# Kernel tuning notes

Measured on AMD Instinct MI355X. Metric: run time of the kernel, lower is better.

## Reference

```python
import jax, jax.numpy as jnp
import numpy as np

D_MODEL = 1024
D_KV = 64
N_HEADS = 16
INNER = N_HEADS * D_KV
EPS = 1e-6


def setup_inputs() -> dict:
    key = jax.random.key(0)
    ks = jax.random.split(key, 8)
    B, SQ, SKV = 2, 2048, 4096
    hidden_states = jax.random.normal(ks[0], (B, SQ, D_MODEL), dtype=jnp.float32)
    key_value_states = jax.random.normal(ks[1], (B, SKV, D_MODEL), dtype=jnp.float32)
    attention_mask = jnp.zeros((B, 1, 1, SKV), dtype=jnp.float32)
    # nn.Linear(in, out, bias=False): y = x @ W.T; store W as [in, out] here
    s = 0.02
    Wq = jax.random.normal(ks[2], (D_MODEL, INNER), dtype=jnp.float32) * s
    Wk = jax.random.normal(ks[3], (D_MODEL, INNER), dtype=jnp.float32) * s
    Wv = jax.random.normal(ks[4], (D_MODEL, INNER), dtype=jnp.float32) * s
    Wo = jax.random.normal(ks[5], (INNER, D_MODEL), dtype=jnp.float32) * s
    ln_weight = jnp.ones((D_MODEL,), dtype=jnp.float32)
    return {
        "hidden_states": hidden_states,
        "key_value_states": key_value_states,
        "attention_mask": attention_mask,
        "ln_weight": ln_weight,
        "Wq": Wq,
        "Wk": Wk,
        "Wv": Wv,
        "Wo": Wo,
    }


def _t5_rmsnorm(x, w, eps=EPS):
    # no mean subtraction, variance in fp32
    var = jnp.mean(jnp.square(x.astype(jnp.float32)), axis=-1, keepdims=True)
    return w * (x * jax.lax.rsqrt(var + eps)).astype(x.dtype)


def reference(hidden_states, key_value_states, attention_mask, ln_weight, Wq, Wk, Wv, Wo):
    B, SQ, _ = hidden_states.shape
    SKV = key_value_states.shape[1]
    normed = _t5_rmsnorm(hidden_states, ln_weight)

    # projections -> [B, H, S, Dk]
    q = (normed @ Wq).reshape(B, SQ, N_HEADS, D_KV).transpose(0, 2, 1, 3)
    k = (key_value_states @ Wk).reshape(B, SKV, N_HEADS, D_KV).transpose(0, 2, 1, 3)
    v = (key_value_states @ Wv).reshape(B, SKV, N_HEADS, D_KV).transpose(0, 2, 1, 3)

    # T5: NO 1/sqrt(d) scaling
    scores = jnp.einsum("bhqd,bhkd->bhqk", q, k) + attention_mask
    attn = jax.nn.softmax(scores.astype(jnp.float32), axis=-1).astype(scores.dtype)
    ctx = jnp.einsum("bhqk,bhkd->bhqd", attn, v)
    ctx = ctx.transpose(0, 2, 1, 3).reshape(B, SQ, INNER)
    attn_out = ctx @ Wo
    return hidden_states + attn_out
```

## Files before the change

### kernel.cpp

```cpp
#include <hip/hip_runtime.h>

typedef unsigned short u16;
typedef unsigned int u32;
typedef __attribute__((ext_vector_type(4))) float f32x4;
typedef __attribute__((ext_vector_type(8))) short short8;
typedef __attribute__((ext_vector_type(4))) short short4v;

#define BB   2
#define SQL  2048
#define SKVL 4096
#define DM   1024
#define NH   16
#define DK   64
#define L2E  1.44269504f

#if __has_builtin(__builtin_amdgcn_exp2f)
#define EXP2(x) __builtin_amdgcn_exp2f(x)
#else
#define EXP2(x) exp2f(x)
#endif

#define MFMA32(a, b, c) __builtin_amdgcn_mfma_f32_16x16x32_bf16(a, b, c, 0, 0, 0)

__device__ __forceinline__ u16 f2bf(float f) {
  union { float f; unsigned u; } v; v.f = f;
  unsigned r = v.u + 0x7fff + ((v.u >> 16) & 1);
  return (u16)(r >> 16);
}

__device__ __forceinline__ short4v pack4(float p0, float p1, float p2, float p3) {
  union { float f; u32 u; } a, b, c, d;
  a.f = p0; b.f = p1; c.f = p2; d.f = p3;
  union { uint2 v; short4v s; } r;
  r.v.x = __builtin_amdgcn_perm(b.u + 0x8000u, a.u + 0x8000u, 0x07060302);
  r.v.y = __builtin_amdgcn_perm(d.u + 0x8000u, c.u + 0x8000u, 0x07060302);
  return r.s;
}

__device__ __forceinline__ void gload16(const void* g, void* lds) {
  __builtin_amdgcn_global_load_lds(
      (const __attribute__((address_space(1))) unsigned int*)g,
      (__attribute__((address_space(3))) unsigned int*)lds, 16, 0, 0);
}

__global__ void pre_kernel(const float* __restrict__ hidden, const float* __restrict__ lnw,
                           const float* __restrict__ kvs,
                           const float* __restrict__ Wq, const float* __restrict__ Wk,
                           const float* __restrict__ Wv, const float* __restrict__ Wo,
                           u16* __restrict__ normed, u16* __restrict__ kvb,
                           u16* __restrict__ Wqt, u16* __restrict__ Wkt,
                           u16* __restrict__ Wvt, u16* __restrict__ Wot) {
  __shared__ float red[4];
  __shared__ float tile[32][33];
  int bid = blockIdx.x, t = threadIdx.x;
  if (bid < 4096) {
    int row = bid;
    float4 v = ((const float4*)(hidden + (size_t)row * DM))[t];
    float ss = v.x * v.x + v.y * v.y + v.z * v.z + v.w * v.w;
#pragma unroll
    for (int m = 32; m >= 1; m >>= 1) ss += __shfl_xor(ss, m, 64);
    int lane = t & 63, wv = t >> 6;
    if (lane == 0) red[wv] = ss;
    __syncthreads();
    float total = red[0] + red[1] + red[2] + red[3];
    float scale = rsqrtf(total * (1.0f / DM) + 1e-6f);
    float4 g = ((const float4*)lnw)[t];
    ushort4 o;
    o.x = f2bf(v.x * scale * g.x);
    o.y = f2bf(v.y * scale * g.y);
    o.z = f2bf(v.z * scale * g.z);
    o.w = f2bf(v.w * scale * g.w);
    ((ushort4*)(normed + (size_t)row * DM))[t] = o;
  } else if (bid < 12288) {
    int i = (bid - 4096) * 256 + t;
    float4 v = ((const float4*)kvs)[i];
    ushort4 o;
    o.x = f2bf(v.x); o.y = f2bf(v.y); o.z = f2bf(v.z); o.w = f2bf(v.w);
    ((ushort4*)kvb)[i] = o;
  } else {
    int g = bid - 12288;
    int z = g >> 10;
    const float* W = (z == 0) ? Wq : (z == 1) ? Wk : (z == 2) ? Wv : Wo;
    u16* Wt = (z == 0) ? Wqt : (z == 1) ? Wkt : (z == 2) ? Wvt : Wot;
    int xx = g & 31, yy = (g >> 5) & 31;
    int tx = t & 31, ty = t >> 5;
    int k0 = yy * 32, n0 = xx * 32;
#pragma unroll
    for (int i = 0; i < 4; i++)
      tile[ty + i * 8][tx] = W[(size_t)(k0 + ty + i * 8) * DM + n0 + tx];
    __syncthreads();
#pragma unroll
    for (int i = 0; i < 4; i++)
      Wt[(size_t)(n0 + ty + i * 8) * DM + k0 + tx] = f2bf(tile[tx][ty + i * 8]);
  }
}

__global__ void proj_kernel(const u16* __restrict__ normed, const u16* __restrict__ kvb,
                            const u16* __restrict__ Wqt, const u16* __restrict__ Wkt,
                            const u16* __restrict__ Wvt,
                            u16* __restrict__ Qb, u16* __restrict__ Kbf,
                            u16* __restrict__ Vtb) {
  const int K = 1024;
  __shared__ __align__(16) u16 Al[128 * 32];
  __shared__ __align__(16) u16 Bl[128 * 32];
  int tid = threadIdx.x, lane = tid & 63, w = tid >> 6;
  int l15 = lane & 15, quad = lane >> 4;
  int wy = w >> 1, wx = w & 1;

  int bid = blockIdx.x;
  int mode;
  const u16 *A, *Bt;
  int tm, tn;
  if (bid < 256) { mode = 0; A = normed; Bt = Wqt; tm = (bid & 31) * 128; tn = (bid >> 5) * 128; }
  else if (bid < 768) { mode = 1; A = kvb; Bt = Wkt; int kid = bid - 256; tm = (kid & 63) * 128; tn = (kid >> 6) * 128; }
  else { mode = 2; A = Wvt; Bt = kvb; int vid = bid - 768; tm = (vid & 7) * 128; tn = (vid >> 3) * 128; }

  f32x4 acc[4][4] = {};
  for (int k0 = 0; k0 < K; k0 += 32) {
    __syncthreads();
#pragma unroll
    for (int r = 0; r < 2; r++) {
      int mg = w * 2 + r;
      gload16(A + (size_t)(tm + mg * 16 + l15) * K + k0 + quad * 8, &Al[mg * 512]);
      gload16(Bt + (size_t)(tn + mg * 16 + l15) * K + k0 + quad * 8, &Bl[mg * 512]);
    }
    __syncthreads();
    short8 af[4], bfr[4];
#pragma unroll
    for (int i = 0; i < 4; i++) {
      af[i] = *(const short8*)&Al[((wy * 4 + i) * 64 + lane) * 8];
      bfr[i] = *(const short8*)&Bl[((wx * 4 + i) * 64 + lane) * 8];
    }
#pragma unroll
    for (int mt = 0; mt < 4; mt++)
#pragma unroll
      for (int nt = 0; nt < 4; nt++)
        acc[mt][nt] = MFMA32(af[mt], bfr[nt], acc[mt][nt]);
  }

#pragma unroll
  for (int mt = 0; mt < 4; mt++) {
    int m0 = tm + wy * 64 + mt * 16 + quad * 4;
#pragma unroll
    for (int nt = 0; nt < 4; nt++) {
      int n = tn + wx * 64 + nt * 16 + l15;
      if (mode == 0) {
#pragma unroll
        for (int r = 0; r < 4; r++)
          Qb[(size_t)(m0 + r) * 1024 + n] = f2bf(acc[mt][nt][r] * L2E);
      } else if (mode == 1) {
#pragma unroll
        for (int r = 0; r < 4; r++)
          Kbf[(size_t)(m0 + r) * 1024 + n] = f2bf(acc[mt][nt][r]);
      } else {
        int b = n >> 12, skv = n & 4095;
        int t32 = skv >> 5, p = skv & 31;
        int s = ((p >> 2) & 3) * 8 + ((p >> 4) & 1) * 4 + (p & 3);
        int h = m0 >> 6, d0 = m0 & 63;
        size_t base = (size_t)((b * NH + h) * 128 + t32) * 2048
                    + (size_t)(d0 >> 4) * 512 + (size_t)(s >> 3) * 128 + (s & 7);
#pragma unroll
        for (int r = 0; r < 4; r++)
          Vtb[base + (size_t)((d0 & 15) + r) * 8] = f2bf(acc[mt][nt][r]);
      }
    }
  }
}

__global__ __launch_bounds__(256, 2) void flash_kernel(
    const u16* __restrict__ Qp, const u16* __restrict__ Kp, const u16* __restrict__ Vtb,
    const float* __restrict__ mask, u16* __restrict__ ctx) {
  __shared__ __align__(16) char smem[65536];
  u16* Kbuf = (u16*)smem;
  u16* Vbuf = (u16*)(smem + 32768);
  float* Ox = (float*)smem;
  float* Ll = (float*)(smem + 32768);

  int tid = threadIdx.x, lane = tid & 63, w = tid >> 6;
  int l15 = lane & 15, quad = lane >> 4;
  int grp = w >> 1, wg = w & 1;

  int lid = blockIdx.y * 16 + blockIdx.x;
  int xcd = lid & 7, slot = lid >> 3;
  int bh = xcd * 4 + (slot >> 4);
  int qb = slot & 15;
  int b = bh >> 4, h = bh & 15;
  int q0 = qb * 128 + wg * 64;

  short8 qf[4][2];
#pragma unroll
  for (int mt = 0; mt < 4; mt++)
#pragma unroll
    for (int kf = 0; kf < 2; kf++)
      qf[mt][kf] = *(const short8*)(Qp + (size_t)(b * SQL + q0 + mt * 16 + l15) * DM +
                                    h * DK + kf * 32 + quad * 8);

  f32x4 of[4][4] = {};
  f32x4 la[4] = {};
  const short8 ones8 = {0x3F80, 0x3F80, 0x3F80, 0x3F80, 0x3F80, 0x3F80, 0x3F80, 0x3F80};

  const size_t vblob = (size_t)(b * NH + h) * 262144;
  const float* mrow = mask + (size_t)b * SKVL;

  auto stage = [&](int tileIdx, int buf) {
    int kv0 = tileIdx * 64;
    u16* Kd = Kbuf + (buf * 2 + grp) * 4096;
    u16* Vd = Vbuf + (buf * 2 + grp) * 4096;
#pragma unroll
    for (int r = 0; r < 4; r++) {
      int u = wg * 4 + r;
      int kt = u >> 1, kf = u & 1;
      gload16(Kp + (size_t)(b * SKVL + kv0 + kt * 16 + l15) * DM + h * DK + kf * 32 + quad * 8,
              &Kd[u * 512]);
      gload16(Vtb + vblob + (size_t)tileIdx * 4096 + u * 512 + lane * 8, &Vd[u * 512]);
    }
  };

  f32x4 mlc[4], mln[4];
  {
    int kv0 = grp * 64;
#pragma unroll
    for (int kt = 0; kt < 4; kt++)
      mlc[kt] = *(const f32x4*)(mrow + kv0 + kt * 16 + quad * 4) * L2E;
  }
  stage(grp, 0);

  union PU { short8 v8; short4v h2[2]; };

  for (int it = 0; it < 32; ++it) {
    __syncthreads();
    if (it + 1 < 32) {
      stage((it + 1) * 2 + grp, (it + 1) & 1);
      int kvn = ((it + 1) * 2 + grp) * 64;
#pragma unroll
      for (int kt = 0; kt < 4; kt++)
        mln[kt] = *(const f32x4*)(mrow + kvn + kt * 16 + quad * 4) * L2E;
    }
    const u16* Kg = Kbuf + ((it & 1) * 2 + grp) * 4096;
    const u16* Vg = Vbuf + ((it & 1) * 2 + grp) * 4096;

#pragma unroll
    for (int ktp = 0; ktp < 2; ktp++) {
      PU paf[4];
#pragma unroll
      for (int kth = 0; kth < 2; kth++) {
        int kt = ktp * 2 + kth;
        short8 k0 = *(const short8*)&Kg[((kt * 2 + 0) * 64 + lane) * 8];
        short8 k1 = *(const short8*)&Kg[((kt * 2 + 1) * 64 + lane) * 8];
#pragma unroll
        for (int mt = 0; mt < 4; mt++) {
          f32x4 st = mlc[kt];
          st = MFMA32(k0, qf[mt][0], st);
          st = MFMA32(k1, qf[mt][1], st);
          paf[mt].h2[kth] = pack4(EXP2(st[0]), EXP2(st[1]), EXP2(st[2]), EXP2(st[3]));
        }
      }
#pragma unroll
      for (int mt = 0; mt < 4; mt++)
        la[mt] = MFMA32(paf[mt].v8, ones8, la[mt]);
#pragma unroll
      for (int nt = 0; nt < 4; nt++) {
        short8 vv = *(const short8*)&Vg[ktp * 2048 + (nt * 64 + lane) * 8];
#pragma unroll
        for (int mt = 0; mt < 4; mt++)
          of[mt][nt] = MFMA32(paf[mt].v8, vv, of[mt][nt]);
      }
    }
#pragma unroll
    for (int kt = 0; kt < 4; kt++) mlc[kt] = mln[kt];
  }

  __syncthreads();
  if (grp == 1) {
#pragma unroll
    for (int mt = 0; mt < 4; mt++) {
#pragma unroll
      for (int nt = 0; nt < 4; nt++)
#pragma unroll
        for (int r = 0; r < 4; r++)
          Ox[(wg * 64 + mt * 16 + quad * 4 + r) * 64 + nt * 16 + l15] = of[mt][nt][r];
      if (l15 == 0)
#pragma unroll
        for (int r = 0; r < 4; r++) Ll[wg * 64 + mt * 16 + quad * 4 + r] = la[mt][r];
    }
  }
  __syncthreads();
  if (grp == 0) {
#pragma unroll
    for (int mt = 0; mt < 4; mt++)
#pragma unroll
      for (int r = 0; r < 4; r++) {
        int ql = wg * 64 + mt * 16 + quad * 4 + r;
        float inv = 1.0f / (la[mt][r] + Ll[ql]);
        int q = qb * 128 + ql;
#pragma unroll
        for (int nt = 0; nt < 4; nt++) {
          float ov = of[mt][nt][r] + Ox[ql * 64 + nt * 16 + l15];
          ctx[(size_t)(b * SQL + q) * DM + h * DK + nt * 16 + l15] = f2bf(ov * inv);
        }
      }
  }
}

__global__ void ogemm_kernel(const u16* __restrict__ A, const u16* __restrict__ Bt,
                             float* __restrict__ C, const float* __restrict__ resid) {
  const int K = 1024;
  __shared__ __align__(16) u16 Al[128 * 32];
  __shared__ __align__(16) u16 Bl[128 * 32];
  int tid = threadIdx.x, lane = tid & 63, w = tid >> 6;
  int l15 = lane & 15, quad = lane >> 4;
  int wy = w >> 1, wx = w & 1;
  int tm = blockIdx.x * 128, tn = blockIdx.y * 128;
  f32x4 acc[4][4] = {};

  for (int k0 = 0; k0 < K; k0 += 32) {
    __syncthreads();
#pragma unroll
    for (int r = 0; r < 2; r++) {
      int mg = w * 2 + r;
      gload16(A + (size_t)(tm + mg * 16 + l15) * K + k0 + quad * 8, &Al[mg * 512]);
      gload16(Bt + (size_t)(tn + mg * 16 + l15) * K + k0 + quad * 8, &Bl[mg * 512]);
    }
    __syncthreads();
    short8 af[4], bfr[4];
#pragma unroll
    for (int i = 0; i < 4; i++) {
      af[i] = *(const short8*)&Al[((wy * 4 + i) * 64 + lane) * 8];
      bfr[i] = *(const short8*)&Bl[((wx * 4 + i) * 64 + lane) * 8];
    }
#pragma unroll
    for (int mt = 0; mt < 4; mt++)
#pragma unroll
      for (int nt = 0; nt < 4; nt++)
        acc[mt][nt] = MFMA32(af[mt], bfr[nt], acc[mt][nt]);
  }

#pragma unroll
  for (int mt = 0; mt < 4; mt++) {
    int m0 = tm + wy * 64 + mt * 16 + quad * 4;
#pragma unroll
    for (int nt = 0; nt < 4; nt++) {
      int n = tn + wx * 64 + nt * 16 + l15;
#pragma unroll
      for (int r = 0; r < 4; r++) {
        size_t idx = (size_t)(m0 + r) * 1024 + n;
        C[idx] = resid[idx] + acc[mt][nt][r];
      }
    }
  }
}

extern "C" void kernel_launch(void* const* d_in, const int* in_sizes, int n_in,
                              void* d_out, int out_size, void* d_ws, size_t ws_size,
                              hipStream_t stream) {
  const float* hidden = (const float*)d_in[0];
  const float* kvs    = (const float*)d_in[1];
  const float* mask   = (const float*)d_in[2];
  const float* lnw    = (const float*)d_in[3];
  const float* Wq     = (const float*)d_in[4];
  const float* Wk     = (const float*)d_in[5];
  const float* Wv     = (const float*)d_in[6];
  const float* Wo     = (const float*)d_in[7];
  char* ws = (char*)d_ws;

  u16* normed = (u16*)(ws + 0);
  u16* kvb    = (u16*)(ws + 8388608);
  u16* Wqt    = (u16*)(ws + 25165824);
  u16* Wkt    = (u16*)(ws + 27262976);
  u16* Wvt    = (u16*)(ws + 29360128);
  u16* Wot    = (u16*)(ws + 31457280);
  u16* Qb     = (u16*)(ws + 33554432);
  u16* Kbf    = (u16*)(ws + 41943040);
  u16* Vtb    = (u16*)(ws + 58720256);
  u16* ctxb   = (u16*)(ws + 75497472);

  pre_kernel<<<16384, 256, 0, stream>>>(hidden, lnw, kvs, Wq, Wk, Wv, Wo,
                                        normed, kvb, Wqt, Wkt, Wvt, Wot);
  proj_kernel<<<1280, 256, 0, stream>>>(normed, kvb, Wqt, Wkt, Wvt, Qb, Kbf, Vtb);
  flash_kernel<<<dim3(SQL / 128, BB * NH), 256, 0, stream>>>(Qb, Kbf, Vtb, mask, ctxb);
  ogemm_kernel<<<dim3(32, 8), 256, 0, stream>>>(ctxb, Wot, (float*)d_out, hidden);
}
```

Measured before the change: 323.6 us.

## Fuse K and V projections sharing A tile, enlarge proj blocks to 512 threads

The projection kernel now computes K and V in the same block, loading each key_value tile once and multiplying it against both Wk and Wv. The V projection is no longer computed as a transposed GEMM, and its output is scattered into the flash layout from the same accumulator positions. Blocks grow to 512 threads with 256x128 tiles for K/V and 128x128 tiles for Q, giving 512 blocks in total. The aim is to halve A-tile traffic for K/V and to reduce the block count. The cost is higher register pressure (two accumulator sets) and uncoalesced scattered V stores.

```diff
diff --git a/kernel.cpp b/kernel.cpp
--- a/kernel.cpp
+++ b/kernel.cpp
@@ -95,73 +95,99 @@
   }
 }
 
-__global__ void proj_kernel(const u16* __restrict__ normed, const u16* __restrict__ kvb,
-                            const u16* __restrict__ Wqt, const u16* __restrict__ Wkt,
-                            const u16* __restrict__ Wvt,
-                            u16* __restrict__ Qb, u16* __restrict__ Kbf,
-                            u16* __restrict__ Vtb) {
+__global__ __launch_bounds__(512, 1) void proj_kernel(
+    const u16* __restrict__ normed, const u16* __restrict__ kvb,
+    const u16* __restrict__ Wqt, const u16* __restrict__ Wkt,
+    const u16* __restrict__ Wvt,
+    u16* __restrict__ Qb, u16* __restrict__ Kbf, u16* __restrict__ Vtb) {
   const int K = 1024;
-  __shared__ __align__(16) u16 Al[128 * 32];
-  __shared__ __align__(16) u16 Bl[128 * 32];
+  __shared__ __align__(16) u16 Al[256 * 32];
+  __shared__ __align__(16) u16 B1[128 * 32];
+  __shared__ __align__(16) u16 B2[128 * 32];
   int tid = threadIdx.x, lane = tid & 63, w = tid >> 6;
   int l15 = lane & 15, quad = lane >> 4;
   int wy = w >> 1, wx = w & 1;
-
   int bid = blockIdx.x;
-  int mode;
-  const u16 *A, *Bt;
-  int tm, tn;
-  if (bid < 256) { mode = 0; A = normed; Bt = Wqt; tm = (bid & 31) * 128; tn = (bid >> 5) * 128; }
-  else if (bid < 768) { mode = 1; A = kvb; Bt = Wkt; int kid = bid - 256; tm = (kid & 63) * 128; tn = (kid >> 6) * 128; }
-  else { mode = 2; A = Wvt; Bt = kvb; int vid = bid - 768; tm = (vid & 7) * 128; tn = (vid >> 3) * 128; }
-
-  f32x4 acc[4][4] = {};
-  for (int k0 = 0; k0 < K; k0 += 32) {
-    __syncthreads();
-#pragma unroll
-    for (int r = 0; r < 2; r++) {
-      int mg = w * 2 + r;
-      gload16(A + (size_t)(tm + mg * 16 + l15) * K + k0 + quad * 8, &Al[mg * 512]);
-      gload16(Bt + (size_t)(tn + mg * 16 + l15) * K + k0 + quad * 8, &Bl[mg * 512]);
-    }
-    __syncthreads();
-    short8 af[4], bfr[4];
-#pragma unroll
-    for (int i = 0; i < 4; i++) {
-      af[i] = *(const short8*)&Al[((wy * 4 + i) * 64 + lane) * 8];
-      bfr[i] = *(const short8*)&Bl[((wx * 4 + i) * 64 + lane) * 8];
-    }
-#pragma unroll
-    for (int mt = 0; mt < 4; mt++)
-#pragma unroll
-      for (int nt = 0; nt < 4; nt++)
-        acc[mt][nt] = MFMA32(af[mt], bfr[nt], acc[mt][nt]);
-  }
-
-#pragma unroll
-  for (int mt = 0; mt < 4; mt++) {
-    int m0 = tm + wy * 64 + mt * 16 + quad * 4;
-#pragma unroll
-    for (int nt = 0; nt < 4; nt++) {
-      int n = tn + wx * 64 + nt * 16 + l15;
-      if (mode == 0) {
+
+  if (bid < 256) {
+    int tm = (bid >> 3) * 256, tn = (bid & 7) * 128;
+    f32x4 ak[4][4] = {}, av[4][4] = {};
+    for (int k0 = 0; k0 < K; k0 += 32) {
+      __syncthreads();
+#pragma unroll
+      for (int r = 0; r < 2; r++) {
+        int mg = w * 2 + r;
+        gload16(kvb + (size_t)(tm + mg * 16 + l15) * K + k0 + quad * 8, &Al[mg * 512]);
+      }
+      gload16(Wkt + (size_t)(tn + w * 16 + l15) * K + k0 + quad * 8, &B1[w * 512]);
+      gload16(Wvt + (size_t)(tn + w * 16 + l15) * K + k0 + quad * 8, &B2[w * 512]);
+      __syncthreads();
+      short8 af[4], bk[4], bv[4];
+#pragma unroll
+      for (int i = 0; i < 4; i++) {
+        af[i] = *(const short8*)&Al[((wy * 4 + i) * 64 + lane) * 8];
+        bk[i] = *(const short8*)&B1[((wx * 4 + i) * 64 + lane) * 8];
+        bv[i] = *(const short8*)&B2[((wx * 4 + i) * 64 + lane) * 8];
+      }
+#pragma unroll
+      for (int mt = 0; mt < 4; mt++)
+#pragma unroll
+        for (int nt = 0; nt < 4; nt++) {
+          ak[mt][nt] = MFMA32(af[mt], bk[nt], ak[mt][nt]);
+          av[mt][nt] = MFMA32(af[mt], bv[nt], av[mt][nt]);
+        }
+    }
+#pragma unroll
+    for (int mt = 0; mt < 4; mt++) {
+      int m0 = tm + wy * 64 + mt * 16 + quad * 4;
+      int bB = m0 >> 12, skv0 = m0 & 4095;
+      int t32 = skv0 >> 5, p0 = skv0 & 31;
+#pragma unroll
+      for (int nt = 0; nt < 4; nt++) {
+        int n = tn + wx * 64 + nt * 16 + l15;
+        int h = n >> 6, d0 = n & 63;
+        size_t vbase = ((size_t)((bB * NH + h) * 128 + t32)) * 2048
+                     + (size_t)(d0 >> 4) * 512 + (size_t)(d0 & 15) * 8;
+#pragma unroll
+        for (int r = 0; r < 4; r++) {
+          Kbf[(size_t)(m0 + r) * 1024 + n] = f2bf(ak[mt][nt][r]);
+          int p = p0 + r;
+          int s = ((p >> 2) & 3) * 8 + ((p >> 4) & 1) * 4 + (p & 3);
+          Vtb[vbase + (s >> 3) * 128 + (s & 7)] = f2bf(av[mt][nt][r]);
+        }
+      }
+    }
+  } else {
+    int qid = bid - 256;
+    int tm = (qid >> 3) * 128, tn = (qid & 7) * 128;
+    f32x4 acc[2][4] = {};
+    for (int k0 = 0; k0 < K; k0 += 32) {
+      __syncthreads();
+      gload16(normed + (size_t)(tm + w * 16 + l15) * K + k0 + quad * 8, &Al[w * 512]);
+      gload16(Wqt + (size_t)(tn + w * 16 + l15) * K + k0 + quad * 8, &B1[w * 512]);
+      __syncthreads();
+      short8 af[2], bfr[4];
+#pragma unroll
+      for (int i = 0; i < 2; i++)
+        af[i] = *(const short8*)&Al[((wy * 2 + i) * 64 + lane) * 8];
+#pragma unroll
+      for (int i = 0; i < 4; i++)
+        bfr[i] = *(const short8*)&B1[((wx * 4 + i) * 64 + lane) * 8];
+#pragma unroll
+      for (int mt = 0; mt < 2; mt++)
+#pragma unroll
+        for (int nt = 0; nt < 4; nt++)
+          acc[mt][nt] = MFMA32(af[mt], bfr[nt], acc[mt][nt]);
+    }
+#pragma unroll
+    for (int mt = 0; mt < 2; mt++) {
+      int m0 = tm + wy * 32 + mt * 16 + quad * 4;
+#pragma unroll
+      for (int nt = 0; nt < 4; nt++) {
+        int n = tn + wx * 64 + nt * 16 + l15;
 #pragma unroll
         for (int r = 0; r < 4; r++)
           Qb[(size_t)(m0 + r) * 1024 + n] = f2bf(acc[mt][nt][r] * L2E);
-      } else if (mode == 1) {
-#pragma unroll
-        for (int r = 0; r < 4; r++)
-          Kbf[(size_t)(m0 + r) * 1024 + n] = f2bf(acc[mt][nt][r]);
-      } else {
-        int b = n >> 12, skv = n & 4095;
-        int t32 = skv >> 5, p = skv & 31;
-        int s = ((p >> 2) & 3) * 8 + ((p >> 4) & 1) * 4 + (p & 3);
-        int h = m0 >> 6, d0 = m0 & 63;
-        size_t base = (size_t)((b * NH + h) * 128 + t32) * 2048
-                    + (size_t)(d0 >> 4) * 512 + (size_t)(s >> 3) * 128 + (s & 7);
-#pragma unroll
-        for (int r = 0; r < 4; r++)
-          Vtb[base + (size_t)((d0 & 15) + r) * 8] = f2bf(acc[mt][nt][r]);
       }
     }
   }
@@ -376,7 +402,7 @@
 
   pre_kernel<<<16384, 256, 0, stream>>>(hidden, lnw, kvs, Wq, Wk, Wv, Wo,
                                         normed, kvb, Wqt, Wkt, Wvt, Wot);
-  proj_kernel<<<1280, 256, 0, stream>>>(normed, kvb, Wqt, Wkt, Wvt, Qb, Kbf, Vtb);
+  proj_kernel<<<512, 512, 0, stream>>>(normed, kvb, Wqt, Wkt, Wvt, Qb, Kbf, Vtb);
   flash_kernel<<<dim3(SQL / 128, BB * NH), 256, 0, stream>>>(Qb, Kbf, Vtb, mask, ctxb);
   ogemm_kernel<<<dim3(32, 8), 256, 0, stream>>>(ctxb, Wot, (float*)d_out, hidden);
 }
```

After: 310.7 us. 4.0% less time.
